# Kernel optimization log

Measured on AMD Instinct MI355X. Metric: run time of the kernel, lower is better.

Reference implementation:

```python
import jax, jax.numpy as jnp
import numpy as np

N_NODES = 10000
N_EDGES = 320000
N_PAIRS = 2048
IN_CH = 128
HIDDEN = 512
OUT_CH = 1

def setup_inputs() -> dict:
    key = jax.random.key(0)
    k = jax.random.split(key, 8)
    x = jax.random.normal(k[0], (N_NODES, IN_CH), dtype=jnp.float32)
    edge_index = jax.random.randint(k[1], (2, N_EDGES), 0, N_NODES, dtype=jnp.int64)
    tar_ei = jax.random.randint(k[2], (2, N_PAIRS), 0, N_NODES, dtype=jnp.int64)
    s1 = 1.0 / np.sqrt(2 * IN_CH)
    s2 = 1.0 / np.sqrt(HIDDEN)
    W1 = jax.random.uniform(k[3], (2 * IN_CH, HIDDEN), jnp.float32, -s1, s1)
    b1 = jax.random.uniform(k[4], (HIDDEN,), jnp.float32, -s1, s1)
    W2 = jax.random.uniform(k[5], (HIDDEN, OUT_CH), jnp.float32, -s2, s2)
    b2 = jax.random.uniform(k[6], (OUT_CH,), jnp.float32, -s2, s2)
    return {"x": x, "edge_index": edge_index, "tar_ei": tar_ei,
            "W1": W1, "b1": b1, "W2": W2, "b2": b2}

def reference(x, edge_index, tar_ei, W1, b1, W2, b2):
    N = x.shape[0]
    # Symmetrized adjacency; coalesce() sums duplicate entries -> scatter-add of ones.
    src = jnp.concatenate([edge_index[0], edge_index[1]])
    dst = jnp.concatenate([edge_index[1], edge_index[0]])
    A = jnp.zeros((N, N), dtype=x.dtype).at[src, dst].add(1.0)  # [N, N]
    ti, tj = tar_ei[0], tar_ei[1]
    Ai = A[ti]  # [B, N] neighbor rows of source endpoints
    Aj = A[tj]  # [B, N] neighbor rows of target endpoints
    # cn_1_1 = Ai * Aj (sparse Hadamard intersection); spmm_add(cn_1_1, x):
    cn_emb = jnp.einsum('bn,bn,nd->bd', Ai, Aj, x)  # [B, in_ch]
    xij = x[ti] * x[tj]                               # [B, in_ch]
    xs = jnp.concatenate([xij, cn_emb], axis=-1)      # [B, 2*in_ch]
    # NOTE: original calls xs.relu() (non in-place) -> no-op, faithfully omitted.
    h = jax.nn.relu(xs @ W1 + b1)
    return h @ W2 + b2
```

## Files before the change

kernel.cpp:

```cpp
#include <hip/hip_runtime.h>

#define N_NODES 10000
#define N_EDGES 320000
#define N_PAIRS 2048
#define IN_CH 128
#define HIDDEN 512
#define PPB 8
#define WIDTH 160
#define NSLOT 4096
#define FBLK (N_PAIRS / PPB)


__global__ __launch_bounds__(256) void k_init(const int* __restrict__ tar,
                                              int* __restrict__ ws) {
    const int t = blockIdx.x * 256 + threadIdx.x;
    if (t >= NSLOT) return;
    ws[10240 + t] = 0;
    ws[tar[t]] = t;
}

__global__ __launch_bounds__(256) void k_edges(const int* __restrict__ ei,
                                               const int* __restrict__ tar,
                                               const int* __restrict__ slotmap,
                                               int* __restrict__ cnt,
                                               unsigned short* __restrict__ adjC) {
    const int e = blockIdx.x * 256 + threadIdx.x;
    if (e >= N_EDGES) return;
    const int s = ei[e];
    const int d = ei[N_EDGES + e];
    int sl = slotmap[s];
    if ((unsigned)sl < (unsigned)NSLOT && tar[sl] == s) {
        const int p = atomicAdd(&cnt[sl], 1);
        if (p < WIDTH) adjC[sl * WIDTH + p] = (unsigned short)d;
    }
    sl = slotmap[d];
    if ((unsigned)sl < (unsigned)NSLOT && tar[sl] == d) {
        const int p = atomicAdd(&cnt[sl], 1);
        if (p < WIDTH) adjC[sl * WIDTH + p] = (unsigned short)s;
    }
}

__global__ __launch_bounds__(256) void k_fused(
    const float* __restrict__ x,
    const int* __restrict__ tar,
    const int* __restrict__ slotmap,
    const int* __restrict__ cnt,
    const unsigned short* __restrict__ adjC,
    const float* __restrict__ W1,
    const float* __restrict__ b1,
    const float* __restrict__ W2,
    const float* __restrict__ b2,
    float* __restrict__ out) {
    const int tid = threadIdx.x;
    __shared__ unsigned short adjJ[PPB][WIDTH];
    __shared__ float sxs[PPB][2 * IN_CH];
    __shared__ float red[PPB][4];

    {
        const int wv = tid >> 6;
        const int lane = tid & 63;
        for (int pi = 0; pi < 2; ++pi) {
            const int p = wv + pi * 4;
            const int pr = blockIdx.x * PPB + p;
            const int ti = tar[pr];
            const int tj = tar[N_PAIRS + pr];
            const int si = slotmap[ti];
            const int sj = slotmap[tj];
            int cj = cnt[sj]; cj = cj < WIDTH ? cj : WIDTH;
            int ci = cnt[si]; ci = ci < WIDTH ? ci : WIDTH;
            for (int q = lane; q < cj; q += 64) adjJ[p][q] = adjC[sj * WIDTH + q];
            float c0 = 0.0f, c1 = 0.0f;
            const int cir = (ci + 63) & ~63;
            for (int pp = lane; pp < cir; pp += 64) {
                const int u = (pp < ci) ? (int)adjC[si * WIDTH + pp] : 0x7FFFFFFF;
                int cm = 0;
                for (int q = 0; q < cj; ++q) cm += ((int)adjJ[p][q] == u) ? 1 : 0;
                unsigned long long m = __ballot(cm > 0);
                while (m) {
                    const int l2 = __ffsll(m) - 1;
                    m &= m - 1;
                    const int uu = __shfl(u, l2, 64);
                    const float fc = (float)__shfl(cm, l2, 64);
                    c0 += fc * x[uu * IN_CH + lane];
                    c1 += fc * x[uu * IN_CH + 64 + lane];
                }
            }
            sxs[p][128 + lane] = c0;
            sxs[p][192 + lane] = c1;
            sxs[p][lane]      = x[ti * IN_CH + lane] * x[tj * IN_CH + lane];
            sxs[p][64 + lane] = x[ti * IN_CH + 64 + lane] * x[tj * IN_CH + 64 + lane];
        }
    }
    __syncthreads();

    const float bja = b1[tid], bjb = b1[tid + 256];
    const float w2a = W2[tid], w2b = W2[tid + 256];
    float acc0[PPB], acc1[PPB];
#pragma unroll
    for (int p = 0; p < PPB; ++p) { acc0[p] = 0.0f; acc1[p] = 0.0f; }
#pragma unroll 8
    for (int k = 0; k < 2 * IN_CH; ++k) {
        const float wa = W1[k * HIDDEN + tid];
        const float wb = W1[k * HIDDEN + tid + 256];
#pragma unroll
        for (int p = 0; p < PPB; ++p) {
            acc0[p] = fmaf(sxs[p][k], wa, acc0[p]);
            acc1[p] = fmaf(sxs[p][k], wb, acc1[p]);
        }
    }
    const int lane = tid & 63;
    const int wv = tid >> 6;
#pragma unroll
    for (int p = 0; p < PPB; ++p) {
        float ha = acc0[p] + bja; ha = ha > 0.0f ? ha : 0.0f;
        float hb = acc1[p] + bjb; hb = hb > 0.0f ? hb : 0.0f;
        float part = ha * w2a + hb * w2b;
        for (int off = 32; off >= 1; off >>= 1)
            part += __shfl_down(part, off, 64);
        if (lane == 0) red[p][wv] = part;
    }
    __syncthreads();
    if (tid < PPB) {
        out[blockIdx.x * PPB + tid] =
            b2[0] + red[tid][0] + red[tid][1] + red[tid][2] + red[tid][3];
    }
}

extern "C" void kernel_launch(void* const* d_in, const int* in_sizes, int n_in,
                              void* d_out, int out_size, void* d_ws, size_t ws_size,
                              hipStream_t stream) {
    const float* x   = (const float*)d_in[0];
    const int*   ei  = (const int*)d_in[1];
    const int*   tar = (const int*)d_in[2];
    const float* W1  = (const float*)d_in[3];
    const float* b1  = (const float*)d_in[4];
    const float* W2  = (const float*)d_in[5];
    const float* b2  = (const float*)d_in[6];
    float* out = (float*)d_out;

    int* ws = (int*)d_ws;
    int* slotmap         = ws;
    int* cnt             = ws + 10240;
    unsigned short* adjC = (unsigned short*)(ws + 14400);

    k_init<<<NSLOT / 256, 256, 0, stream>>>(tar, ws);
    k_edges<<<(N_EDGES + 255) / 256, 256, 0, stream>>>(ei, tar, slotmap, cnt, adjC);
    k_fused<<<FBLK, 256, 0, stream>>>(x, tar, slotmap, cnt, adjC, W1, b1, W2, b2, out);
}
```

Baseline: 114.7 us.

## Pad atomic counters, split edge directions across threads, widen fused block to 512

Counters are spread out by a stride of 16 ints so that atomics on different slots stop hitting the same cache lines. The edge kernel now uses one thread per directed edge instead of one per undirected edge handling both directions. The fused kernel runs 512 threads per block, giving each wave one pair and each thread one hidden unit, and x rows are loaded as float2. In exchange, each thread carries fewer accumulators, the workspace grows, and twice as many edge threads are launched.

```diff
diff --git a/kernel.cpp b/kernel.cpp
--- a/kernel.cpp
+++ b/kernel.cpp
@@ -8,6 +8,7 @@
 #define PPB 8
 #define WIDTH 160
 #define NSLOT 4096
+#define CSTRIDE 16
 #define FBLK (N_PAIRS / PPB)
 
 
@@ -15,7 +16,7 @@
                                               int* __restrict__ ws) {
     const int t = blockIdx.x * 256 + threadIdx.x;
     if (t >= NSLOT) return;
-    ws[10240 + t] = 0;
+    ws[10240 + t * CSTRIDE] = 0;
     ws[tar[t]] = t;
 }
 
@@ -24,23 +25,18 @@
                                                const int* __restrict__ slotmap,
                                                int* __restrict__ cnt,
                                                unsigned short* __restrict__ adjC) {
-    const int e = blockIdx.x * 256 + threadIdx.x;
-    if (e >= N_EDGES) return;
-    const int s = ei[e];
-    const int d = ei[N_EDGES + e];
-    int sl = slotmap[s];
-    if ((unsigned)sl < (unsigned)NSLOT && tar[sl] == s) {
-        const int p = atomicAdd(&cnt[sl], 1);
-        if (p < WIDTH) adjC[sl * WIDTH + p] = (unsigned short)d;
-    }
-    sl = slotmap[d];
-    if ((unsigned)sl < (unsigned)NSLOT && tar[sl] == d) {
-        const int p = atomicAdd(&cnt[sl], 1);
-        if (p < WIDTH) adjC[sl * WIDTH + p] = (unsigned short)s;
+    const int k = blockIdx.x * 256 + threadIdx.x;
+    if (k >= 2 * N_EDGES) return;
+    const int from = ei[k];
+    const int to = (k >= N_EDGES) ? ei[k - N_EDGES] : ei[k + N_EDGES];
+    const int sl = slotmap[from];
+    if ((unsigned)sl < (unsigned)NSLOT && tar[sl] == from) {
+        const int p = atomicAdd(&cnt[sl * CSTRIDE], 1);
+        if (p < WIDTH) adjC[sl * WIDTH + p] = (unsigned short)to;
     }
 }
 
-__global__ __launch_bounds__(256) void k_fused(
+__global__ __launch_bounds__(512) void k_fused(
     const float* __restrict__ x,
     const int* __restrict__ tar,
     const int* __restrict__ slotmap,
@@ -54,75 +50,70 @@
     const int tid = threadIdx.x;
     __shared__ unsigned short adjJ[PPB][WIDTH];
     __shared__ float sxs[PPB][2 * IN_CH];
-    __shared__ float red[PPB][4];
+    __shared__ float red[PPB][8];
 
     {
-        const int wv = tid >> 6;
+        const int p = tid >> 6;
         const int lane = tid & 63;
-        for (int pi = 0; pi < 2; ++pi) {
-            const int p = wv + pi * 4;
-            const int pr = blockIdx.x * PPB + p;
-            const int ti = tar[pr];
-            const int tj = tar[N_PAIRS + pr];
-            const int si = slotmap[ti];
-            const int sj = slotmap[tj];
-            int cj = cnt[sj]; cj = cj < WIDTH ? cj : WIDTH;
-            int ci = cnt[si]; ci = ci < WIDTH ? ci : WIDTH;
-            for (int q = lane; q < cj; q += 64) adjJ[p][q] = adjC[sj * WIDTH + q];
-            float c0 = 0.0f, c1 = 0.0f;
-            const int cir = (ci + 63) & ~63;
-            for (int pp = lane; pp < cir; pp += 64) {
-                const int u = (pp < ci) ? (int)adjC[si * WIDTH + pp] : 0x7FFFFFFF;
-                int cm = 0;
-                for (int q = 0; q < cj; ++q) cm += ((int)adjJ[p][q] == u) ? 1 : 0;
-                unsigned long long m = __ballot(cm > 0);
-                while (m) {
-                    const int l2 = __ffsll(m) - 1;
-                    m &= m - 1;
-                    const int uu = __shfl(u, l2, 64);
-                    const float fc = (float)__shfl(cm, l2, 64);
-                    c0 += fc * x[uu * IN_CH + lane];
-                    c1 += fc * x[uu * IN_CH + 64 + lane];
-                }
+        const int pr = blockIdx.x * PPB + p;
+        const int ti = tar[pr];
+        const int tj = tar[N_PAIRS + pr];
+        const float2 xi = ((const float2*)(x + ti * IN_CH))[lane];
+        const float2 xj = ((const float2*)(x + tj * IN_CH))[lane];
+        const int si = slotmap[ti];
+        const int sj = slotmap[tj];
+        int cj = cnt[sj * CSTRIDE]; cj = cj < WIDTH ? cj : WIDTH;
+        int ci = cnt[si * CSTRIDE]; ci = ci < WIDTH ? ci : WIDTH;
+        for (int q = lane; q < cj; q += 64) adjJ[p][q] = adjC[sj * WIDTH + q];
+        float2 c2 = {0.0f, 0.0f};
+        const int cir = (ci + 63) & ~63;
+        for (int pp = lane; pp < cir; pp += 64) {
+            const int u = (pp < ci) ? (int)adjC[si * WIDTH + pp] : 0x7FFFFFFF;
+            int cm = 0;
+            for (int q = 0; q < cj; ++q) cm += ((int)adjJ[p][q] == u) ? 1 : 0;
+            unsigned long long m = __ballot(cm > 0);
+            while (m) {
+                const int l2 = __ffsll(m) - 1;
+                m &= m - 1;
+                const int uu = __shfl(u, l2, 64);
+                const float fc = (float)__shfl(cm, l2, 64);
+                const float2 xu = ((const float2*)(x + uu * IN_CH))[lane];
+                c2.x += fc * xu.x;
+                c2.y += fc * xu.y;
             }
-            sxs[p][128 + lane] = c0;
-            sxs[p][192 + lane] = c1;
-            sxs[p][lane]      = x[ti * IN_CH + lane] * x[tj * IN_CH + lane];
-            sxs[p][64 + lane] = x[ti * IN_CH + 64 + lane] * x[tj * IN_CH + 64 + lane];
         }
+        ((float2*)&sxs[p][0])[lane]     = make_float2(xi.x * xj.x, xi.y * xj.y);
+        ((float2*)&sxs[p][IN_CH])[lane] = c2;
     }
     __syncthreads();
 
-    const float bja = b1[tid], bjb = b1[tid + 256];
-    const float w2a = W2[tid], w2b = W2[tid + 256];
-    float acc0[PPB], acc1[PPB];
+    const float bj = b1[tid];
+    const float w2 = W2[tid];
+    float acc[PPB];
 #pragma unroll
-    for (int p = 0; p < PPB; ++p) { acc0[p] = 0.0f; acc1[p] = 0.0f; }
+    for (int p = 0; p < PPB; ++p) acc[p] = 0.0f;
 #pragma unroll 8
     for (int k = 0; k < 2 * IN_CH; ++k) {
-        const float wa = W1[k * HIDDEN + tid];
-        const float wb = W1[k * HIDDEN + tid + 256];
+        const float w = W1[k * HIDDEN + tid];
 #pragma unroll
-        for (int p = 0; p < PPB; ++p) {
-            acc0[p] = fmaf(sxs[p][k], wa, acc0[p]);
-            acc1[p] = fmaf(sxs[p][k], wb, acc1[p]);
-        }
+        for (int p = 0; p < PPB; ++p) acc[p] = fmaf(sxs[p][k], w, acc[p]);
     }
     const int lane = tid & 63;
     const int wv = tid >> 6;
 #pragma unroll
     for (int p = 0; p < PPB; ++p) {
-        float ha = acc0[p] + bja; ha = ha > 0.0f ? ha : 0.0f;
-        float hb = acc1[p] + bjb; hb = hb > 0.0f ? hb : 0.0f;
-        float part = ha * w2a + hb * w2b;
+        float h = acc[p] + bj; h = h > 0.0f ? h : 0.0f;
+        float part = h * w2;
         for (int off = 32; off >= 1; off >>= 1)
             part += __shfl_down(part, off, 64);
         if (lane == 0) red[p][wv] = part;
     }
     __syncthreads();
     if (tid < PPB) {
-        out[blockIdx.x * PPB + tid] =
-            b2[0] + red[tid][0] + red[tid][1] + red[tid][2] + red[tid][3];
+        float s = b2[0];
+#pragma unroll
+        for (int w = 0; w < 8; ++w) s += red[tid][w];
+        out[blockIdx.x * PPB + tid] = s;
     }
 }
 
@@ -141,9 +132,9 @@
     int* ws = (int*)d_ws;
     int* slotmap         = ws;
     int* cnt             = ws + 10240;
-    unsigned short* adjC = (unsigned short*)(ws + 14400);
+    unsigned short* adjC = (unsigned short*)(ws + 75776);
 
     k_init<<<NSLOT / 256, 256, 0, stream>>>(tar, ws);
-    k_edges<<<(N_EDGES + 255) / 256, 256, 0, stream>>>(ei, tar, slotmap, cnt, adjC);
-    k_fused<<<FBLK, 256, 0, stream>>>(x, tar, slotmap, cnt, adjC, W1, b1, W2, b2, out);
+    k_edges<<<(2 * N_EDGES + 255) / 256, 256, 0, stream>>>(ei, tar, slotmap, cnt, adjC);
+    k_fused<<<FBLK, 512, 0, stream>>>(x, tar, slotmap, cnt, adjC, W1, b1, W2, b2, out);
 }
```

Measured after the change: 104.0 us. 1.1x faster.
